# Optimization experiments

Measured on AMD Instinct MI355X. Metric: run time of the kernel, lower is better.

The kernel has to match this reference:

```python
import jax, jax.numpy as jnp
import numpy as np

B, N, K = 8, 1024, 16        # graphs, points per graph, kNN fan-in (loop=True includes self)
LATENT = 256
EPS = 1e-5                   # PyG BatchNorm eps


def _bn(x, g, b):
    # training-mode batch norm over all leading (node/edge) dims, per channel
    ax = tuple(range(x.ndim - 1))
    mu = jnp.mean(x, axis=ax, keepdims=True)
    var = jnp.var(x, axis=ax, keepdims=True)
    return g * (x - mu) * jax.lax.rsqrt(var + EPS) + b


def setup_inputs() -> dict:
    key = jax.random.key(0)
    ks = jax.random.split(key, 12)

    def lin(k, fi, fo):
        s = (6.0 / (fi + fo)) ** 0.5
        kw, kb = jax.random.split(k)
        W = jax.random.uniform(kw, (fi, fo), jnp.float32, -s, s)
        bb = jax.random.uniform(kb, (fo,), jnp.float32, -s, s)
        return W, bb

    pos = jax.random.normal(ks[0], (B * N, 3), jnp.float32)
    batch = jnp.repeat(jnp.arange(B, dtype=jnp.int32), N)

    c1_W1, c1_b1 = lin(ks[1], 6, 64)
    c1_W2, c1_b2 = lin(ks[2], 64, 64)
    c2_W1, c2_b1 = lin(ks[3], 67, 64)
    c2_W2, c2_b2 = lin(ks[4], 64, 128)
    c2_W3, c2_b3 = lin(ks[5], 128, 1024)
    lin_W, lin_b = lin(ks[6], 1024, LATENT)

    return {
        "pos": pos, "batch": batch,
        "c1_W1": c1_W1, "c1_b1": c1_b1,
        "c1_g1": jnp.ones((64,), jnp.float32), "c1_be1": jnp.zeros((64,), jnp.float32),
        "c1_W2": c1_W2, "c1_b2": c1_b2,
        "c2_W1": c2_W1, "c2_b1": c2_b1,
        "c2_g1": jnp.ones((64,), jnp.float32), "c2_be1": jnp.zeros((64,), jnp.float32),
        "c2_W2": c2_W2, "c2_b2": c2_b2,
        "c2_g2": jnp.ones((128,), jnp.float32), "c2_be2": jnp.zeros((128,), jnp.float32),
        "c2_W3": c2_W3, "c2_b3": c2_b3,
        "lin_W": lin_W, "lin_b": lin_b,
        "lin_g": jnp.ones((LATENT,), jnp.float32), "lin_be": jnp.zeros((LATENT,), jnp.float32),
    }


def reference(pos, batch,
              c1_W1, c1_b1, c1_g1, c1_be1, c1_W2, c1_b2,
              c2_W1, c2_b1, c2_g1, c2_be1, c2_W2, c2_b2,
              c2_g2, c2_be2, c2_W3, c2_b3,
              lin_W, lin_b, lin_g, lin_be):
    # ---- kNN graph (per-graph, loop=True: self is nearest) ----
    p3 = pos.reshape(B, N, 3)
    sq = jnp.sum(p3 * p3, axis=-1)                                   # [B,N]
    d = sq[:, :, None] + sq[:, None, :] - 2.0 * jnp.einsum('bnd,bmd->bnm', p3, p3)
    _, nbr = jax.lax.top_k(-d, K)                                    # [B,N,K] neighbor ids
    idx = (nbr + (jnp.arange(B) * N)[:, None, None]).reshape(B * N, K)

    # ---- PointNetConv 1: gather -> MLP([6,64,64]) -> max aggregate ----
    pj = pos[idx]                                                    # [P,K,3]
    rel = pj - pos[:, None, :]                                       # [P,K,3]
    feat = jnp.concatenate([pj, rel], axis=-1)                       # [P,K,6]
    h = jax.nn.relu(_bn(feat @ c1_W1 + c1_b1, c1_g1, c1_be1))
    x1 = jnp.max(h @ c1_W2 + c1_b2, axis=1)                          # [P,64]

    # ---- PointNetConv 2: MLP([67,64,128,1024]) -> max aggregate ----
    feat2 = jnp.concatenate([x1[idx], rel], axis=-1)                 # [P,K,67]
    h = jax.nn.relu(_bn(feat2 @ c2_W1 + c2_b1, c2_g1, c2_be1))
    h = jax.nn.relu(_bn(h @ c2_W2 + c2_b2, c2_g2, c2_be2))
    x2 = jnp.max(h @ c2_W3 + c2_b3, axis=1)                          # [P,1024]

    # ---- global max pool per graph + final MLP (plain_last=False) ----
    g = x2.reshape(B, N, -1).max(axis=1)                             # [B,1024]
    return jax.nn.relu(_bn(g @ lin_W + lin_b, lin_g, lin_be))        # [B,LATENT]
```

## Files before the change

kernel.cpp:

```cpp
#include <hip/hip_runtime.h>
#include <math.h>

#define NB   8
#define NPTS 1024
#define PTS  8192
#define KNN  16
#define PK   (PTS*KNN)

typedef __attribute__((ext_vector_type(8))) _Float16 f16x8;
typedef __attribute__((ext_vector_type(4))) float f32x4;

__device__ __forceinline__ unsigned short f2h(float f) {
  _Float16 h = (_Float16)f;
  union { _Float16 h; unsigned short u; } c; c.h = h;
  return c.u;
}
__device__ __forceinline__ float h2f(unsigned short u) {
  union { unsigned short u; _Float16 h; } c; c.u = u;
  return (float)c.h;
}
__device__ __forceinline__ int lanerank(unsigned long long m) {
  return __builtin_amdgcn_mbcnt_hi((unsigned)(m >> 32),
         __builtin_amdgcn_mbcnt_lo((unsigned)m, 0));
}

__global__ __launch_bounds__(256) void knn_conv1_kernel(const float* __restrict__ pos,
    const float* __restrict__ W1, const float* __restrict__ b1,
    int* __restrict__ idx, float* __restrict__ rel,
    unsigned short* __restrict__ z1h, float* __restrict__ mid1) {
  __shared__ float px[NPTS], py[NPTS], pz[NPTS];
  __shared__ float feat[4][KNN][6];
  __shared__ float ls[256], ls2[256];
  const int t = threadIdx.x;
  const int wv = t >> 6, lane = t & 63;
  const int b = blockIdx.x;
  const int graph = b >> 8;
  const int base = graph << 10;
  for (int j = t; j < NPTS; j += 256) {
    px[j] = pos[3*(base+j)];
    py[j] = pos[3*(base+j)+1];
    pz[j] = pos[3*(base+j)+2];
  }
  __syncthreads();

  const int il = ((b & 255) << 2) + wv;
  const int i  = base + il;
  const float pix = px[il], piy = py[il], piz = pz[il];
  const float sqi = pix*pix + piy*piy + piz*piz;

  unsigned key[16];
  #pragma unroll
  for (int q = 0; q < 16; ++q) {
    const int j = (q << 6) + lane;
    const float x = px[j], y = py[j], z = pz[j];
    const float sqj = x*x + y*y + z*z;
    const float dt  = pix*x + piy*y + piz*z;
    const float d   = sqi + sqj - 2.0f*dt;
    const unsigned db = __float_as_uint(d);
    key[q] = (db >> 31) ? ~db : (db | 0x80000000u);
  }

  unsigned V = 0;
  #pragma unroll 1
  for (int bb = 31; bb >= 0; --bb) {
    const unsigned test = V | (1u << bb);
    int cnt = 0;
    #pragma unroll
    for (int q = 0; q < 16; ++q)
      cnt += __popcll(__ballot(key[q] < test));
    if (cnt < 16) V = test;
  }

  int c = 0;
  #pragma unroll
  for (int q = 0; q < 16; ++q)
    c += __popcll(__ballot(key[q] < V));

  int p_lt = 0, p_eq = c;
  #pragma unroll 1
  for (int q = 0; q < 16; ++q) {
    const unsigned long long mlt = __ballot(key[q] < V);
    const unsigned long long meq = __ballot(key[q] == V);
    int slot = -1;
    if (key[q] < V) slot = p_lt + lanerank(mlt);
    else if (key[q] == V) {
      const int s = p_eq + lanerank(meq);
      if (s < 16) slot = s;
    }
    if (slot >= 0) {
      const int j = (q << 6) + lane;
      const int r = i*KNN + slot;
      const float rx = px[j] - pix, ry = py[j] - piy, rz = pz[j] - piz;
      idx[r] = base + j;
      rel[3*r] = rx; rel[3*r+1] = ry; rel[3*r+2] = rz;
      feat[wv][slot][0] = px[j]; feat[wv][slot][1] = py[j]; feat[wv][slot][2] = pz[j];
      feat[wv][slot][3] = rx;    feat[wv][slot][4] = ry;    feat[wv][slot][5] = rz;
    }
    p_lt += __popcll(mlt);
    p_eq += __popcll(meq);
  }

  float w[6];
  #pragma unroll
  for (int q = 0; q < 6; ++q) w[q] = W1[q*64 + lane];
  const float bbv = b1[lane];
  float s = 0.0f, s2 = 0.0f;
  #pragma unroll
  for (int k = 0; k < KNN; ++k) {
    float z = bbv;
    #pragma unroll
    for (int q = 0; q < 6; ++q) z += feat[wv][k][q]*w[q];
    z1h[(size_t)(i*KNN + k)*64 + lane] = f2h(z);
    s += z; s2 += z*z;
  }
  ls[t] = s; ls2[t] = s2;
  __syncthreads();
  if (t < 64) {
    float a  = ls[t] + ls[t+64] + ls[t+128] + ls[t+192];
    float a2 = ls2[t] + ls2[t+64] + ls2[t+128] + ls2[t+192];
    const int cp = (b & 7) * 128;
    atomicAdd(&mid1[cp + t], a);
    atomicAdd(&mid1[cp + 64 + t], a2);
  }
}

__global__ __launch_bounds__(256) void wprep_kernel(const float* __restrict__ W3,
    const float* __restrict__ W2, const float* __restrict__ W1c2,
    const float* __restrict__ W2c1,
    unsigned short* __restrict__ W3T, unsigned short* __restrict__ W2T,
    unsigned short* __restrict__ w1T, unsigned short* __restrict__ W2c1T) {
  const int b = blockIdx.x, t = threadIdx.x;
  if (b < 128) {
    const int k = b;
    const int ks = k >> 5, qd = (k >> 3) & 3, e = k & 7;
    for (int n = t; n < 1024; n += 256) {
      const int nb = n >> 4, mc = n & 15;
      W3T[((nb*4 + ks) << 9) + qd*128 + mc*8 + e] = f2h(W3[(size_t)k*1024 + n]);
    }
  } else if (b < 132) {
    for (int id = (b-128)*2048 + t; id < (b-127)*2048; id += 256) {
      const int n = id >> 6, k = id & 63;
      W2T[n*64 + k] = f2h(W2[k*128 + n]);
    }
  } else if (b < 136) {
    for (int id = (b-132)*1024 + t; id < (b-131)*1024; id += 256) {
      const int n = id >> 6, k = id & 63;
      w1T[n*64 + k] = f2h(W1c2[k*64 + n]);
    }
  } else {
    for (int id = (b-136)*1024 + t; id < (b-135)*1024; id += 256) {
      const int n = id >> 6, k = id & 63;
      W2c1T[n*64 + k] = f2h(W2c1[k*64 + n]);
    }
  }
}

__global__ __launch_bounds__(256) void conv1_l2max_mfma(
    const unsigned short* __restrict__ z1h, const float* __restrict__ mid1,
    const float* __restrict__ g1, const float* __restrict__ be1,
    const unsigned short* __restrict__ W2T, const float* __restrict__ b2,
    unsigned short* __restrict__ x1h) {
  __shared__ unsigned short As[128*64];
  __shared__ float scl[64], shl[64];
  const int r0 = blockIdx.x * 128;
  const int t = threadIdx.x;
  const int lane = t & 63, w = t >> 6;
  const int quad = lane >> 4, mcol = lane & 15;
  const float invR = 1.0f / (float)PK;

  if (t < 64) {
    float s = 0.0f, s2 = 0.0f;
    #pragma unroll
    for (int k = 0; k < 8; ++k) { s += mid1[k*128 + t]; s2 += mid1[k*128 + 64 + t]; }
    const float mu  = s * invR;
    const float var = s2 * invR - mu*mu;
    const float sc  = g1[t] * rsqrtf(var + 1e-5f);
    scl[t] = sc; shl[t] = be1[t] - mu*sc;
  }
  __syncthreads();

  {
    const int kb = t & 7, rr = t >> 3;
    float sc[8], sh[8];
    #pragma unroll
    for (int q = 0; q < 8; ++q) { sc[q] = scl[kb*8 + q]; sh[q] = shl[kb*8 + q]; }
    #pragma unroll
    for (int it = 0; it < 4; ++it) {
      const int r = rr + it*32;
      union { uint4 v; unsigned short s[8]; } in;
      in.v = *(const uint4*)(z1h + (size_t)(r0 + r)*64 + kb*8);
      union { unsigned short s[8]; uint4 v; } o;
      #pragma unroll
      for (int q = 0; q < 8; ++q)
        o.s[q] = f2h(fmaxf(h2f(in.s[q])*sc[q] + sh[q], 0.0f));
      *(uint4*)(As + r*64 + ((kb ^ (r & 7)) * 8)) = o.v;
    }
  }
  __syncthreads();

  const int wrow = (w >> 1) * 64;
  const int wncol = (w & 1) * 32;

  f32x4 acc[4][2];
  #pragma unroll
  for (int mi = 0; mi < 4; ++mi)
    #pragma unroll
    for (int ni = 0; ni < 2; ++ni)
      acc[mi][ni] = (f32x4){0.f, 0.f, 0.f, 0.f};

  #pragma unroll
  for (int ks = 0; ks < 2; ++ks) {
    f16x8 af[4], bfr[2];
    #pragma unroll
    for (int mi = 0; mi < 4; ++mi) {
      const int row = wrow + mi*16 + mcol;
      af[mi] = *(const f16x8*)(As + row*64 + (((ks*4 + quad) ^ (row & 7)) * 8));
    }
    #pragma unroll
    for (int ni = 0; ni < 2; ++ni) {
      const int nr = wncol + ni*16 + mcol;
      bfr[ni] = *(const f16x8*)(W2T + nr*64 + ks*32 + quad*8);
    }
    #pragma unroll
    for (int mi = 0; mi < 4; ++mi)
      #pragma unroll
      for (int ni = 0; ni < 2; ++ni)
        acc[mi][ni] = __builtin_amdgcn_mfma_f32_16x16x32_f16(af[mi], bfr[ni], acc[mi][ni], 0, 0, 0);
  }

  float bb[2];
  #pragma unroll
  for (int ni = 0; ni < 2; ++ni) bb[ni] = b2[wncol + ni*16 + mcol];
  #pragma unroll
  for (int mi = 0; mi < 4; ++mi) {
    const int p = blockIdx.x*8 + (w >> 1)*4 + mi;
    #pragma unroll
    for (int ni = 0; ni < 2; ++ni) {
      f32x4 a = acc[mi][ni];
      float m = fmaxf(fmaxf(a[0], a[1]), fmaxf(a[2], a[3]));
      m = fmaxf(m, __shfl_xor(m, 16));
      m = fmaxf(m, __shfl_xor(m, 32));
      if (quad == 0) x1h[(size_t)p*64 + wncol + ni*16 + mcol] = f2h(m + bb[ni]);
    }
  }
}

__global__ __launch_bounds__(256) void conv2_l1_mfma(
    const unsigned short* __restrict__ x1h, const int* __restrict__ idx,
    const float* __restrict__ rel, const unsigned short* __restrict__ w1T,
    const float* __restrict__ W1full, const float* __restrict__ b1,
    unsigned short* __restrict__ zah, float* __restrict__ midA) {
  __shared__ unsigned short S[128*64];
  __shared__ int   idxr[128];
  __shared__ float rl[128*3];
  __shared__ float ps[256];
  const int r0 = blockIdx.x * 128;
  const int t = threadIdx.x;
  const int lane = t & 63, w = t >> 6;
  const int quad = lane >> 4, mcol = lane & 15;

  if (t < 128) idxr[t] = idx[r0 + t];
  else if (t < 224) *(float4*)(rl + (t-128)*4) = *(const float4*)(rel + (size_t)r0*3 + (t-128)*4);
  __syncthreads();

  {
    const int kb = t & 7, rr = t >> 3;
    #pragma unroll
    for (int it = 0; it < 4; ++it) {
      const int r = rr + it*32;
      const int gj = idxr[r];
      const uint4 v = *(const uint4*)(x1h + (size_t)gj*64 + kb*8);
      *(uint4*)(S + r*64 + ((kb ^ (r & 7)) * 8)) = v;
    }
  }
  __syncthreads();

  const int wrow = (w >> 1) * 64;
  const int wcol = (w & 1) * 32;

  f16x8 af[2][4], bfr[2][2];
  #pragma unroll
  for (int ks = 0; ks < 2; ++ks)
    #pragma unroll
    for (int mi = 0; mi < 4; ++mi) {
      const int row = wrow + mi*16 + mcol;
      af[ks][mi] = *(const f16x8*)(S + row*64 + (((ks*4 + quad) ^ (row & 7)) * 8));
    }
  #pragma unroll
  for (int ks = 0; ks < 2; ++ks)
    #pragma unroll
    for (int ni = 0; ni < 2; ++ni) {
      const int nr = wcol + ni*16 + mcol;
      bfr[ks][ni] = *(const f16x8*)(w1T + nr*64 + ks*32 + quad*8);
    }

  f32x4 acc[4][2];
  #pragma unroll
  for (int mi = 0; mi < 4; ++mi)
    #pragma unroll
    for (int ni = 0; ni < 2; ++ni)
      acc[mi][ni] = (f32x4){0.f, 0.f, 0.f, 0.f};

  #pragma unroll
  for (int ks = 0; ks < 2; ++ks)
    #pragma unroll
    for (int mi = 0; mi < 4; ++mi)
      #pragma unroll
      for (int ni = 0; ni < 2; ++ni)
        acc[mi][ni] = __builtin_amdgcn_mfma_f32_16x16x32_f16(af[ks][mi], bfr[ks][ni], acc[mi][ni], 0, 0, 0);

  __syncthreads();

  float bb[2], wr0[2], wr1[2], wr2[2];
  #pragma unroll
  for (int ni = 0; ni < 2; ++ni) {
    const int col = wcol + ni*16 + mcol;
    bb[ni]  = b1[col];
    wr0[ni] = W1full[64*64 + col];
    wr1[ni] = W1full[65*64 + col];
    wr2[ni] = W1full[66*64 + col];
  }
  float s[2] = {0,0}, s2[2] = {0,0};
  #pragma unroll
  for (int mi = 0; mi < 4; ++mi) {
    #pragma unroll
    for (int j = 0; j < 4; ++j) {
      const int row = wrow + mi*16 + quad*4 + j;
      const float r0v = rl[row*3], r1v = rl[row*3+1], r2v = rl[row*3+2];
      #pragma unroll
      for (int ni = 0; ni < 2; ++ni) {
        const int col = wcol + ni*16 + mcol;
        const int g = col >> 3, o = col & 7;
        const float v = acc[mi][ni][j] + bb[ni] + r0v*wr0[ni] + r1v*wr1[ni] + r2v*wr2[ni];
        S[row*64 + ((g ^ (row & 7)) << 3) + o] = f2h(v);
        s[ni] += v; s2[ni] += v*v;
      }
    }
  }
  #pragma unroll
  for (int ni = 0; ni < 2; ++ni) {
    s[ni]  += __shfl_xor(s[ni], 16);  s[ni]  += __shfl_xor(s[ni], 32);
    s2[ni] += __shfl_xor(s2[ni], 16); s2[ni] += __shfl_xor(s2[ni], 32);
  }
  if (quad == 0) {
    const int rh = w >> 1;
    #pragma unroll
    for (int ni = 0; ni < 2; ++ni) {
      const int col = wcol + ni*16 + mcol;
      ps[rh*128 + col]      = s[ni];
      ps[rh*128 + 64 + col] = s2[ni];
    }
  }
  __syncthreads();

  #pragma unroll
  for (int i = 0; i < 4; ++i) {
    const int u = i*256 + t;
    const int row = u >> 3, gg = u & 7;
    *(uint4*)(zah + (size_t)(r0 + row)*64 + gg*8) =
        *(const uint4*)(S + row*64 + ((gg ^ (row & 7)) << 3));
  }
  if (t < 128) atomicAdd(&midA[(blockIdx.x & 7)*128 + t], ps[t] + ps[128 + t]);
}

__global__ __launch_bounds__(256) void conv2_l2_mfma(
    const unsigned short* __restrict__ zah, const float* __restrict__ midA,
    const float* __restrict__ g1, const float* __restrict__ be1,
    const unsigned short* __restrict__ W2T, const float* __restrict__ b2,
    unsigned short* __restrict__ zhb, float* __restrict__ midB) {
  __shared__ unsigned short S[128*128];
  __shared__ float ps[512];
  __shared__ float scl[64], shl[64];
  const int r0 = blockIdx.x * 128;
  const int t = threadIdx.x;
  const int lane = t & 63, w = t >> 6;
  const int quad = lane >> 4, mcol = lane & 15;
  const float invR = 1.0f / (float)PK;

  if (t < 64) {
    float s = 0.0f, s2 = 0.0f;
    #pragma unroll
    for (int k = 0; k < 8; ++k) { s += midA[k*128 + t]; s2 += midA[k*128 + 64 + t]; }
    const float mu  = s * invR;
    const float var = s2 * invR - mu*mu;
    const float sc  = g1[t] * rsqrtf(var + 1e-5f);
    scl[t] = sc; shl[t] = be1[t] - mu*sc;
  }
  __syncthreads();

  {
    const int kb = t & 7, rr = t >> 3;
    float sc[8], sh[8];
    #pragma unroll
    for (int q = 0; q < 8; ++q) { sc[q] = scl[kb*8 + q]; sh[q] = shl[kb*8 + q]; }
    #pragma unroll
    for (int it = 0; it < 4; ++it) {
      const int r = rr + it*32;
      union { uint4 v; unsigned short s[8]; } in;
      in.v = *(const uint4*)(zah + (size_t)(r0 + r)*64 + kb*8);
      union { unsigned short s[8]; uint4 v; } o;
      #pragma unroll
      for (int q = 0; q < 8; ++q)
        o.s[q] = f2h(fmaxf(h2f(in.s[q])*sc[q] + sh[q], 0.0f));
      *(uint4*)(S + r*64 + ((kb ^ (r & 7)) * 8)) = o.v;
    }
  }
  __syncthreads();

  const int wrow = (w >> 1) * 64;
  const int wcol = (w & 1) * 64;

  f16x8 af[2][4], bfr[2][4];
  #pragma unroll
  for (int ks = 0; ks < 2; ++ks)
    #pragma unroll
    for (int mi = 0; mi < 4; ++mi) {
      const int row = wrow + mi*16 + mcol;
      af[ks][mi] = *(const f16x8*)(S + row*64 + (((ks*4 + quad) ^ (row & 7)) * 8));
    }
  #pragma unroll
  for (int ks = 0; ks < 2; ++ks)
    #pragma unroll
    for (int ni = 0; ni < 4; ++ni) {
      const int nr = wcol + ni*16 + mcol;
      bfr[ks][ni] = *(const f16x8*)(W2T + nr*64 + ks*32 + quad*8);
    }

  f32x4 acc[4][4];
  #pragma unroll
  for (int mi = 0; mi < 4; ++mi)
    #pragma unroll
    for (int ni = 0; ni < 4; ++ni)
      acc[mi][ni] = (f32x4){0.f, 0.f, 0.f, 0.f};

  #pragma unroll
  for (int ks = 0; ks < 2; ++ks)
    #pragma unroll
    for (int mi = 0; mi < 4; ++mi)
      #pragma unroll
      for (int ni = 0; ni < 4; ++ni)
        acc[mi][ni] = __builtin_amdgcn_mfma_f32_16x16x32_f16(af[ks][mi], bfr[ks][ni], acc[mi][ni], 0, 0, 0);

  __syncthreads();

  float bb[4];
  #pragma unroll
  for (int ni = 0; ni < 4; ++ni) bb[ni] = b2[wcol + ni*16 + mcol];
  float s[4] = {0,0,0,0}, s2[4] = {0,0,0,0};
  #pragma unroll
  for (int mi = 0; mi < 4; ++mi) {
    #pragma unroll
    for (int ni = 0; ni < 4; ++ni) {
      const int col = wcol + ni*16 + mcol;
      const int g = col >> 3, o = col & 7;
      #pragma unroll
      for (int j = 0; j < 4; ++j) {
        const int row = wrow + mi*16 + quad*4 + j;
        const float v = acc[mi][ni][j] + bb[ni];
        S[row*128 + ((g ^ (row & 15)) << 3) + o] = f2h(v);
        s[ni] += v; s2[ni] += v*v;
      }
    }
  }
  #pragma unroll
  for (int ni = 0; ni < 4; ++ni) {
    s[ni]  += __shfl_xor(s[ni], 16);  s[ni]  += __shfl_xor(s[ni], 32);
    s2[ni] += __shfl_xor(s2[ni], 16); s2[ni] += __shfl_xor(s2[ni], 32);
  }
  if (quad == 0) {
    const int rh = w >> 1;
    #pragma unroll
    for (int ni = 0; ni < 4; ++ni) {
      const int col = wcol + ni*16 + mcol;
      ps[rh*256 + col]       = s[ni];
      ps[rh*256 + 128 + col] = s2[ni];
    }
  }
  __syncthreads();

  #pragma unroll
  for (int i = 0; i < 8; ++i) {
    const int u = i*256 + t;
    const int row = u >> 4, gg = u & 15;
    *(uint4*)(zhb + (size_t)(r0 + row)*128 + gg*8) =
        *(const uint4*)(S + row*128 + ((gg ^ (row & 15)) << 3));
  }
  atomicAdd(&midB[(blockIdx.x & 7)*256 + t], ps[t] + ps[256 + t]);
}

__global__ __launch_bounds__(256, 3) void conv2_l3max_mfma(
    const unsigned short* __restrict__ zhb, const float* __restrict__ midB,
    const float* __restrict__ g2, const float* __restrict__ be2,
    const unsigned short* __restrict__ W3T,
    float* __restrict__ pmax2) {
  __shared__ unsigned short As[128*128];
  __shared__ float pm[1024];
  __shared__ float scl[128], shl[128];
  const int rb = blockIdx.x & 1023, ch = blockIdx.x >> 10;
  const int r0 = rb * 128;
  const int t = threadIdx.x;
  const int lane = t & 63, w = t >> 6;
  const int quad = lane >> 4, mcol = lane & 15;
  const float invR = 1.0f / (float)PK;

  #pragma unroll
  for (int i = 0; i < 4; ++i) pm[i*256 + t] = -INFINITY;

  if (t < 128) {
    float s = 0.0f, s2 = 0.0f;
    #pragma unroll
    for (int k = 0; k < 8; ++k) { s += midB[k*256 + t]; s2 += midB[k*256 + 128 + t]; }
    const float mu  = s * invR;
    const float var = s2 * invR - mu*mu;
    const float sc  = g2[t] * rsqrtf(var + 1e-5f);
    scl[t] = sc; shl[t] = be2[t] - mu*sc;
  }
  __syncthreads();

  {
    const int kb = t & 15, rr = t >> 4;
    float sc[8], sh[8];
    #pragma unroll
    for (int q = 0; q < 8; ++q) { sc[q] = scl[kb*8 + q]; sh[q] = shl[kb*8 + q]; }
    #pragma unroll
    for (int it = 0; it < 8; ++it) {
      const int r = rr + it*16;
      union { uint4 v; unsigned short s[8]; } in;
      in.v = *(const uint4*)(zhb + (size_t)(r0 + r)*128 + kb*8);
      union { unsigned short s[8]; uint4 v; } o;
      #pragma unroll
      for (int q = 0; q < 8; ++q)
        o.s[q] = f2h(fmaxf(h2f(in.s[q])*sc[q] + sh[q], 0.0f));
      *(uint4*)(As + r*128 + ((kb ^ (r & 7)) * 8)) = o.v;
    }
  }
  __syncthreads();

  const int wrow = (w >> 1) * 64;
  const int wncol = (w & 1) * 32;
  const int rh = w >> 1;

  #pragma unroll 1
  for (int chunk = 0; chunk < 8; ++chunk) {
    const int nb0 = ch*32 + chunk*4 + (w & 1)*2;

    f32x4 acc[4][2];
    #pragma unroll
    for (int mi = 0; mi < 4; ++mi)
      #pragma unroll
      for (int ni = 0; ni < 2; ++ni)
        acc[mi][ni] = (f32x4){0.f, 0.f, 0.f, 0.f};

    #pragma unroll
    for (int ks = 0; ks < 4; ++ks) {
      f16x8 bfr[2], af[4];
      #pragma unroll
      for (int ni = 0; ni < 2; ++ni)
        bfr[ni] = *(const f16x8*)(W3T + (((nb0 + ni)*4 + ks) << 9) + lane*8);
      #pragma unroll
      for (int mi = 0; mi < 4; ++mi) {
        const int row = wrow + mi*16 + mcol;
        af[mi] = *(const f16x8*)(As + row*128 + (((ks*4 + quad) ^ (row & 7)) * 8));
      }
      #pragma unroll
      for (int mi = 0; mi < 4; ++mi)
        #pragma unroll
        for (int ni = 0; ni < 2; ++ni)
          acc[mi][ni] = __builtin_amdgcn_mfma_f32_16x16x32_f16(af[mi], bfr[ni], acc[mi][ni], 0, 0, 0);
    }

    #pragma unroll
    for (int ni = 0; ni < 2; ++ni) {
      float m4 = -INFINITY;
      #pragma unroll
      for (int mi = 0; mi < 4; ++mi) {
        f32x4 a = acc[mi][ni];
        m4 = fmaxf(m4, fmaxf(fmaxf(a[0], a[1]), fmaxf(a[2], a[3])));
      }
      m4 = fmaxf(m4, __shfl_xor(m4, 16));
      m4 = fmaxf(m4, __shfl_xor(m4, 32));
      if (quad == 0) {
        const int pc = rh*512 + chunk*64 + wncol + ni*16 + mcol;
        pm[pc] = fmaxf(pm[pc], m4);
      }
    }
  }
  __syncthreads();

  pmax2[(size_t)rb*1024 + ch*512 + t]       = fmaxf(pm[t], pm[512 + t]);
  pmax2[(size_t)rb*1024 + ch*512 + 256 + t] = fmaxf(pm[256 + t], pm[768 + t]);
}

__global__ __launch_bounds__(256) void pool_final_kernel(const float* __restrict__ pmax2,
    const float* __restrict__ b3, float* __restrict__ g) {
  const int b = blockIdx.x >> 2, q = blockIdx.x & 3;
  const int c = q*256 + threadIdx.x;
  const float* p = pmax2 + (size_t)b*128*1024 + c;
  float m = -INFINITY;
  for (int rb = 0; rb < 128; ++rb) m = fmaxf(m, p[(size_t)rb*1024]);
  g[b*1024 + c] = m + b3[c];
}

__global__ __launch_bounds__(256) void lin_kernel(const float* __restrict__ g,
    const float* __restrict__ W, float* __restrict__ zpart) {
  const int b = blockIdx.x >> 2, q = blockIdx.x & 3;
  const int o = threadIdx.x;
  const float* gb = g + b*1024 + q*256;
  const float* Wq = W + q*256*256;
  float acc = 0.0f;
  for (int c = 0; c < 256; ++c) acc += gb[c] * Wq[c*256 + o];
  zpart[blockIdx.x*256 + o] = acc;
}

__global__ __launch_bounds__(256) void final_kernel(const float* __restrict__ zpart,
    const float* __restrict__ lb, const float* __restrict__ lg,
    const float* __restrict__ lbe, float* __restrict__ out) {
  const int o = threadIdx.x;
  float z[NB]; float s = 0.0f, s2 = 0.0f;
  #pragma unroll
  for (int b = 0; b < NB; ++b) {
    float v = lb[o];
    #pragma unroll
    for (int q = 0; q < 4; ++q) v += zpart[(b*4+q)*256 + o];
    z[b] = v; s += v; s2 += v*v;
  }
  const float mu  = s * 0.125f;
  const float var = s2 * 0.125f - mu*mu;
  const float inv = rsqrtf(var + 1e-5f);
  const float sc = lg[o]*inv, sh = lbe[o] - mu*sc;
  #pragma unroll
  for (int b = 0; b < NB; ++b) out[b*256 + o] = fmaxf(z[b]*sc + sh, 0.0f);
}

extern "C" void kernel_launch(void* const* d_in, const int* in_sizes, int n_in,
                              void* d_out, int out_size, void* d_ws, size_t ws_size,
                              hipStream_t stream) {
  const float* pos    = (const float*)d_in[0];
  const float* c1_W1  = (const float*)d_in[2];
  const float* c1_b1  = (const float*)d_in[3];
  const float* c1_g1  = (const float*)d_in[4];
  const float* c1_be1 = (const float*)d_in[5];
  const float* c1_W2  = (const float*)d_in[6];
  const float* c1_b2  = (const float*)d_in[7];
  const float* c2_W1  = (const float*)d_in[8];
  const float* c2_b1  = (const float*)d_in[9];
  const float* c2_g1  = (const float*)d_in[10];
  const float* c2_be1 = (const float*)d_in[11];
  const float* c2_W2  = (const float*)d_in[12];
  const float* c2_b2  = (const float*)d_in[13];
  const float* c2_g2  = (const float*)d_in[14];
  const float* c2_be2 = (const float*)d_in[15];
  const float* c2_W3  = (const float*)d_in[16];
  const float* c2_b3  = (const float*)d_in[17];
  const float* lin_W  = (const float*)d_in[18];
  const float* lin_b  = (const float*)d_in[19];
  const float* lin_g  = (const float*)d_in[20];
  const float* lin_be = (const float*)d_in[21];
  float* out = (float*)d_out;

  char* ws = (char*)d_ws;
  int*   idx     = (int*)  (ws + 0);
  float* rel     = (float*)(ws + 524288);
  float* zpart   = (float*)(ws + 2097152 + 2048);
  float* gpool   = (float*)(ws + 2097152 + 2048 + 32768);
  float* mid1    = (float*)(ws + 2164736);
  float* midA    = (float*)(ws + 2164736 + 4096);
  float* midB    = (float*)(ws + 2164736 + 8192);
  unsigned short* W2T   = (unsigned short*)(ws + 2295808);
  unsigned short* w1T   = (unsigned short*)(ws + 2312192);
  unsigned short* W2c1T = (unsigned short*)(ws + 2320384);
  unsigned short* z1h = (unsigned short*)(ws + 2426880);
  unsigned short* zah = (unsigned short*)(ws + 2426880);
  float* pmax2   = (float*)(ws + 2426880);
  unsigned short* x1h = (unsigned short*)(ws + 35981312);
  unsigned short* zhb = (unsigned short*)(ws + 38078464);
  unsigned short* W3T = (unsigned short*)(ws + 71632896);

  hipMemsetAsync(ws + 2164736, 0, 16384, stream);
  wprep_kernel<<<140, 256, 0, stream>>>(c2_W3, c2_W2, c2_W1, c1_W2, W3T, W2T, w1T, W2c1T);
  knn_conv1_kernel<<<PTS/4, 256, 0, stream>>>(pos, c1_W1, c1_b1, idx, rel, z1h, mid1);
  conv1_l2max_mfma<<<PK/128, 256, 0, stream>>>(z1h, mid1, c1_g1, c1_be1, W2c1T, c1_b2, x1h);
  conv2_l1_mfma<<<PK/128, 256, 0, stream>>>(x1h, idx, rel, w1T, c2_W1, c2_b1, zah, midA);
  conv2_l2_mfma<<<PK/128, 256, 0, stream>>>(zah, midA, c2_g1, c2_be1, W2T, c2_b2, zhb, midB);
  conv2_l3max_mfma<<<PK/64, 256, 0, stream>>>(zhb, midB, c2_g2, c2_be2, W3T, pmax2);
  pool_final_kernel<<<NB*4, 256, 0, stream>>>(pmax2, c2_b3, gpool);
  lin_kernel<<<32, 256, 0, stream>>>(gpool, lin_W, zpart);
  final_kernel<<<1, 256, 0, stream>>>(zpart, lin_b, lin_g, lin_be, out);
}
```

Before: 236.0 us.

## Merge conv2 layer-3 column halves per block, fuse pool with lin, fold memset

The layer-3 max kernel now has each 128-row block compute all 1024 output columns instead of splitting them across two blocks. The normalised activation tile is therefore built once per row block, not twice. The pooling and final linear kernels are merged into one kernel that keeps the pooled vector in shared memory, and the workspace memset becomes an extra block of the weight-prep kernel, which removes two launches. The cost is half as many blocks in the heaviest kernel, so less parallelism and longer per-block serial chunks, and the stats buffer is now zeroed inside a kernel.

```diff
diff --git a/kernel.cpp b/kernel.cpp
--- a/kernel.cpp
+++ b/kernel.cpp
@@ -128,7 +128,8 @@
     const float* __restrict__ W2, const float* __restrict__ W1c2,
     const float* __restrict__ W2c1,
     unsigned short* __restrict__ W3T, unsigned short* __restrict__ W2T,
-    unsigned short* __restrict__ w1T, unsigned short* __restrict__ W2c1T) {
+    unsigned short* __restrict__ w1T, unsigned short* __restrict__ W2c1T,
+    float* __restrict__ mids) {
   const int b = blockIdx.x, t = threadIdx.x;
   if (b < 128) {
     const int k = b;
@@ -147,11 +148,13 @@
       const int n = id >> 6, k = id & 63;
       w1T[n*64 + k] = f2h(W1c2[k*64 + n]);
     }
-  } else {
+  } else if (b < 140) {
     for (int id = (b-136)*1024 + t; id < (b-135)*1024; id += 256) {
       const int n = id >> 6, k = id & 63;
       W2c1T[n*64 + k] = f2h(W2c1[k*64 + n]);
     }
+  } else {
+    for (int i2 = t; i2 < 4096; i2 += 256) mids[i2] = 0.0f;
   }
 }
 
@@ -494,18 +497,16 @@
     const unsigned short* __restrict__ W3T,
     float* __restrict__ pmax2) {
   __shared__ unsigned short As[128*128];
-  __shared__ float pm[1024];
-  __shared__ float scl[128], shl[128];
-  const int rb = blockIdx.x & 1023, ch = blockIdx.x >> 10;
+  __shared__ float pm[2048];
+  float* const scl = pm;
+  float* const shl = pm + 128;
+  const int rb = blockIdx.x;
   const int r0 = rb * 128;
   const int t = threadIdx.x;
   const int lane = t & 63, w = t >> 6;
   const int quad = lane >> 4, mcol = lane & 15;
   const float invR = 1.0f / (float)PK;
 
-  #pragma unroll
-  for (int i = 0; i < 4; ++i) pm[i*256 + t] = -INFINITY;
-
   if (t < 128) {
     float s = 0.0f, s2 = 0.0f;
     #pragma unroll
@@ -541,8 +542,8 @@
   const int rh = w >> 1;
 
   #pragma unroll 1
-  for (int chunk = 0; chunk < 8; ++chunk) {
-    const int nb0 = ch*32 + chunk*4 + (w & 1)*2;
+  for (int chunk = 0; chunk < 16; ++chunk) {
+    const int nb0 = chunk*4 + (w & 1)*2;
 
     f32x4 acc[4][2];
     #pragma unroll
@@ -579,37 +580,36 @@
       }
       m4 = fmaxf(m4, __shfl_xor(m4, 16));
       m4 = fmaxf(m4, __shfl_xor(m4, 32));
-      if (quad == 0) {
-        const int pc = rh*512 + chunk*64 + wncol + ni*16 + mcol;
-        pm[pc] = fmaxf(pm[pc], m4);
-      }
-    }
-  }
-  __syncthreads();
-
-  pmax2[(size_t)rb*1024 + ch*512 + t]       = fmaxf(pm[t], pm[512 + t]);
-  pmax2[(size_t)rb*1024 + ch*512 + 256 + t] = fmaxf(pm[256 + t], pm[768 + t]);
-}
-
-__global__ __launch_bounds__(256) void pool_final_kernel(const float* __restrict__ pmax2,
-    const float* __restrict__ b3, float* __restrict__ g) {
+      if (quad == 0)
+        pm[rh*1024 + chunk*64 + wncol + ni*16 + mcol] = m4;
+    }
+  }
+  __syncthreads();
+
+  #pragma unroll
+  for (int i = 0; i < 4; ++i) {
+    const int c = i*256 + t;
+    pmax2[(size_t)rb*1024 + c] = fmaxf(pm[c], pm[1024 + c]);
+  }
+}
+
+__global__ __launch_bounds__(256) void poollin_kernel(const float* __restrict__ pmax2,
+    const float* __restrict__ b3, const float* __restrict__ W,
+    float* __restrict__ zpart) {
+  __shared__ float gs[256];
   const int b = blockIdx.x >> 2, q = blockIdx.x & 3;
-  const int c = q*256 + threadIdx.x;
+  const int t = threadIdx.x;
+  const int c = q*256 + t;
   const float* p = pmax2 + (size_t)b*128*1024 + c;
   float m = -INFINITY;
+  #pragma unroll 4
   for (int rb = 0; rb < 128; ++rb) m = fmaxf(m, p[(size_t)rb*1024]);
-  g[b*1024 + c] = m + b3[c];
-}
-
-__global__ __launch_bounds__(256) void lin_kernel(const float* __restrict__ g,
-    const float* __restrict__ W, float* __restrict__ zpart) {
-  const int b = blockIdx.x >> 2, q = blockIdx.x & 3;
-  const int o = threadIdx.x;
-  const float* gb = g + b*1024 + q*256;
-  const float* Wq = W + q*256*256;
+  gs[t] = m + b3[c];
+  __syncthreads();
+  const float* Wq = W + (size_t)q*256*256;
   float acc = 0.0f;
-  for (int c = 0; c < 256; ++c) acc += gb[c] * Wq[c*256 + o];
-  zpart[blockIdx.x*256 + o] = acc;
+  for (int cc = 0; cc < 256; ++cc) acc += gs[cc] * Wq[cc*256 + t];
+  zpart[blockIdx.x*256 + t] = acc;
 }
 
 __global__ __launch_bounds__(256) void final_kernel(const float* __restrict__ zpart,
@@ -662,7 +662,6 @@
   int*   idx     = (int*)  (ws + 0);
   float* rel     = (float*)(ws + 524288);
   float* zpart   = (float*)(ws + 2097152 + 2048);
-  float* gpool   = (float*)(ws + 2097152 + 2048 + 32768);
   float* mid1    = (float*)(ws + 2164736);
   float* midA    = (float*)(ws + 2164736 + 4096);
   float* midB    = (float*)(ws + 2164736 + 8192);
@@ -676,14 +675,12 @@
   unsigned short* zhb = (unsigned short*)(ws + 38078464);
   unsigned short* W3T = (unsigned short*)(ws + 71632896);
 
-  hipMemsetAsync(ws + 2164736, 0, 16384, stream);
-  wprep_kernel<<<140, 256, 0, stream>>>(c2_W3, c2_W2, c2_W1, c1_W2, W3T, W2T, w1T, W2c1T);
+  wprep_kernel<<<141, 256, 0, stream>>>(c2_W3, c2_W2, c2_W1, c1_W2, W3T, W2T, w1T, W2c1T, mid1);
   knn_conv1_kernel<<<PTS/4, 256, 0, stream>>>(pos, c1_W1, c1_b1, idx, rel, z1h, mid1);
   conv1_l2max_mfma<<<PK/128, 256, 0, stream>>>(z1h, mid1, c1_g1, c1_be1, W2c1T, c1_b2, x1h);
   conv2_l1_mfma<<<PK/128, 256, 0, stream>>>(x1h, idx, rel, w1T, c2_W1, c2_b1, zah, midA);
   conv2_l2_mfma<<<PK/128, 256, 0, stream>>>(zah, midA, c2_g1, c2_be1, W2T, c2_b2, zhb, midB);
-  conv2_l3max_mfma<<<PK/64, 256, 0, stream>>>(zhb, midB, c2_g2, c2_be2, W3T, pmax2);
-  pool_final_kernel<<<NB*4, 256, 0, stream>>>(pmax2, c2_b3, gpool);
-  lin_kernel<<<32, 256, 0, stream>>>(gpool, lin_W, zpart);
+  conv2_l3max_mfma<<<PK/128, 256, 0, stream>>>(zhb, midB, c2_g2, c2_be2, W3T, pmax2);
+  poollin_kernel<<<NB*4, 256, 0, stream>>>(pmax2, c2_b3, lin_W, zpart);
   final_kernel<<<1, 256, 0, stream>>>(zpart, lin_b, lin_g, lin_be, out);
 }
```

Measured after the change: 228.3 us. 1.03x faster.
